# Performance work log

Hardware: AMD Instinct MI355X
Metric: run time of the kernel (lower is better)

Reference implementation:

```python
import jax, jax.numpy as jnp
import numpy as np

D_MODEL = 1024
N_HEADS = 16
D_HEAD = D_MODEL // N_HEADS
RANK = 128
N_COMPRESS = 64
STATE_DIM = 64
B_SZ = 2
S_LEN = 2048


def setup_inputs() -> dict:
    key = jax.random.key(0)
    ks = jax.random.split(key, 12)
    x = jax.random.normal(ks[0], (B_SZ, S_LEN, D_MODEL), dtype=jnp.float32)
    A = jax.random.normal(ks[1], (STATE_DIM, STATE_DIM), dtype=jnp.float32) * 0.01
    B_ssm = jax.random.normal(ks[2], (D_MODEL, STATE_DIM), dtype=jnp.float32) * 0.01
    W_imp = jax.random.normal(ks[3], (D_MODEL, STATE_DIM), dtype=jnp.float32) * 0.02   # Linear(state_dim->d_model), weight [out,in]
    W_router = jax.random.normal(ks[4], (N_COMPRESS, D_MODEL), dtype=jnp.float32) * 0.02
    compress_neurons = jax.random.normal(ks[5], (N_COMPRESS, D_MODEL, RANK), dtype=jnp.float32) * 0.02
    Wq = jax.random.normal(ks[6], (D_MODEL, RANK), dtype=jnp.float32) * 0.02
    Wk = jax.random.normal(ks[7], (D_MODEL, RANK), dtype=jnp.float32) * 0.02
    Wv = jax.random.normal(ks[8], (D_MODEL, RANK), dtype=jnp.float32) * 0.02
    Wo = jax.random.normal(ks[9], (D_MODEL, D_MODEL), dtype=jnp.float32) * 0.02
    mask = jnp.tril(jnp.ones((S_LEN, S_LEN), dtype=bool))[None, None]  # [1,1,S,S] causal
    return {"x": x, "A": A, "B_ssm": B_ssm, "W_imp": W_imp, "W_router": W_router,
            "compress_neurons": compress_neurons, "Wq": Wq, "Wk": Wk, "Wv": Wv,
            "Wo": Wo, "mask": mask}


def reference(x, A, B_ssm, W_imp, W_router, compress_neurons, Wq, Wk, Wv, Wo, mask):
    Bn, S, D = x.shape
    # ---- SSM: h_t = h_{t-1} @ A + x_t @ B (only final state is used) ----
    xB = jnp.einsum('bsd,dn->bsn', x, B_ssm)  # precompute input projection

    def step(h, u):
        h = h @ A + u
        return h, None

    h0 = jnp.zeros((Bn, STATE_DIM), dtype=x.dtype)
    h_final, _ = jax.lax.scan(step, h0, jnp.swapaxes(xB, 0, 1))  # scan over S

    h_proj = h_final @ W_imp.T                       # [B, d_model]
    importance = jax.nn.softmax(jnp.einsum('bsd,bd->bs', x, h_proj), axis=-1)

    # ---- Routing ----
    token_pref = jax.nn.softmax(x @ W_router.T, axis=-1)          # [B,S,n_compress]
    nw = jnp.einsum('bs,bsn->bn', importance, token_pref)         # [B,n_compress]
    nw = nw / (nw.sum(axis=-1, keepdims=True) + 1e-8)

    # ---- Shared compression -> QKV ----
    shared_compress = jnp.einsum('bn,ndr->bdr', nw, compress_neurons)  # [B,D,rank]
    hcomp = jnp.einsum('bsd,bdr->bsr', x, shared_compress)             # [B,S,rank]
    Q = (hcomp @ Wq.T).reshape(Bn, S, N_HEADS, D_HEAD).transpose(0, 2, 1, 3)
    K = (hcomp @ Wk.T).reshape(Bn, S, N_HEADS, D_HEAD).transpose(0, 2, 1, 3)
    V = (hcomp @ Wv.T).reshape(Bn, S, N_HEADS, D_HEAD).transpose(0, 2, 1, 3)

    scores = jnp.einsum('bhqd,bhkd->bhqk', Q, K) / np.sqrt(D_HEAD).astype(x.dtype)
    scores = jnp.where(mask, scores, jnp.array(-jnp.inf, dtype=scores.dtype))
    attn = jax.nn.softmax(scores, axis=-1)
    attn_out = jnp.einsum('bhqk,bhkd->bhqd', attn, V)
    attn_out = attn_out.transpose(0, 2, 1, 3).reshape(Bn, S, D_MODEL)
    output = attn_out @ Wo.T
    return output
```

## Files before the change

### kernel.cpp

```cpp
#include <hip/hip_runtime.h>
#include <hip/hip_bf16.h>

typedef __bf16 bf16x8 __attribute__((ext_vector_type(8)));
typedef float  f32x4  __attribute__((ext_vector_type(4)));
typedef float  f32x16 __attribute__((ext_vector_type(16)));
typedef unsigned int uint4v __attribute__((ext_vector_type(4)));

__device__ __forceinline__ unsigned short f2bf(float f){
  union { float f; unsigned int u; } v; v.f = f;
  unsigned int r = (v.u + 0x7FFFu + ((v.u >> 16) & 1u)) >> 16;
  return (unsigned short)r;
}

__device__ __forceinline__ float bf2f(unsigned short u){
  union { unsigned int i; float f; } v; v.i = ((unsigned int)u) << 16; return v.f;
}

__device__ __forceinline__ unsigned pkbf(float a, float b){
  unsigned r;
  asm("v_cvt_pk_bf16_f32 %0, %1, %2" : "=v"(r) : "v"(a), "v"(b));
  return r;
}

__device__ __forceinline__ void gload_lds16(const void* g, void* l){
  __builtin_amdgcn_global_load_lds(
      (const __attribute__((address_space(1))) unsigned int*)g,
      (__attribute__((address_space(3))) unsigned int*)l, 16, 0, 0);
}

#define MFMA16(a,b,c) __builtin_amdgcn_mfma_f32_16x16x32_bf16((a),(b),(c),0,0,0)
#define MFMA32(a,b,c) __builtin_amdgcn_mfma_f32_32x32x16_bf16((a),(b),(c),0,0,0)

__global__ void k_conv(const float* __restrict__ x,
                       const float* __restrict__ Wq, const float* __restrict__ Wk,
                       const float* __restrict__ Wv, const float* __restrict__ Wo,
                       const float* __restrict__ Wr,
                       unsigned short* __restrict__ xb16,
                       unsigned short* __restrict__ wqkv, unsigned short* __restrict__ wo,
                       unsigned short* __restrict__ wrt){
  int bid = blockIdx.x;
  if (bid < 4096){
    int i = (bid * 256 + threadIdx.x) * 4;
    float4 v = *reinterpret_cast<const float4*>(x + i);
    ushort4 r; r.x = f2bf(v.x); r.y = f2bf(v.y); r.z = f2bf(v.z); r.w = f2bf(v.w);
    *reinterpret_cast<ushort4*>(xb16 + i) = r;
    return;
  }
  int j = ((bid - 4096) * 256 + threadIdx.x) * 4;
  if (j < 393216){
    const float* s;
    if (j < 131072) s = Wq + j; else if (j < 262144) s = Wk + (j - 131072); else s = Wv + (j - 262144);
    float4 v = *reinterpret_cast<const float4*>(s);
    ushort4 r; r.x = f2bf(v.x); r.y = f2bf(v.y); r.z = f2bf(v.z); r.w = f2bf(v.w);
    *reinterpret_cast<ushort4*>(wqkv + j) = r;
  } else if (j < 1441792){
    int jj = j - 393216;
    float4 v = *reinterpret_cast<const float4*>(Wo + jj);
    ushort4 r; r.x = f2bf(v.x); r.y = f2bf(v.y); r.z = f2bf(v.z); r.w = f2bf(v.w);
    *reinterpret_cast<ushort4*>(wo + jj) = r;
  } else {
    int jj = j - 1441792;
    int n = jj >> 10, d = jj & 1023;
    ushort4 r;
    if (n < 64){
      float4 v = *reinterpret_cast<const float4*>(Wr + n * 1024 + d);
      r.x = f2bf(v.x); r.y = f2bf(v.y); r.z = f2bf(v.z); r.w = f2bf(v.w);
    } else { r.x = 0; r.y = 0; r.z = 0; r.w = 0; }
    *reinterpret_cast<ushort4*>(wrt + jj) = r;
  }
}

template<int CBF16>
__global__ __launch_bounds__(256) void k_gemm(
    const unsigned short* __restrict__ A, const unsigned short* __restrict__ Bt,
    void* __restrict__ Cv, int M, int N, int K,
    long sA, long sB, long sC)
{
  __shared__ __align__(16) unsigned short Al[128 * 64];
  __shared__ __align__(16) unsigned short Bl[128 * 64];
  const int tid = threadIdx.x, wv = tid >> 6, lane = tid & 63;
  const int bm = blockIdx.y * 128, bn = blockIdx.x * 128, z = blockIdx.z;
  const unsigned short* Ab = A + (long)z * sA;
  const unsigned short* Bb = Bt + (long)z * sB;
  const f32x4 zero = {0.f, 0.f, 0.f, 0.f};
  f32x4 acc[4][4];
  #pragma unroll
  for (int i = 0; i < 4; ++i)
    #pragma unroll
    for (int j = 0; j < 4; ++j) acc[i][j] = zero;
  const int mo = (wv & 1) * 64, no = (wv >> 1) * 64;

  for (int k0 = 0; k0 < K; k0 += 64){
    __syncthreads();
    #pragma unroll
    for (int i = 0; i < 4; ++i){
      int rr = (wv * 4 + i) * 8 + (lane >> 3);
      gload_lds16(Ab + (long)(bm + rr) * K + k0 + (lane & 7) * 8, &Al[(wv * 4 + i) * 8 * 64]);
      gload_lds16(Bb + (long)(bn + rr) * K + k0 + (lane & 7) * 8, &Bl[(wv * 4 + i) * 8 * 64]);
    }
    __syncthreads();
    #pragma unroll
    for (int ks = 0; ks < 2; ++ks){
      bf16x8 af[4], bfr[4];
      #pragma unroll
      for (int mi = 0; mi < 4; ++mi)
        af[mi] = *reinterpret_cast<const bf16x8*>(&Al[(mo + mi * 16 + (lane & 15)) * 64 + ks * 32 + (lane >> 4) * 8]);
      #pragma unroll
      for (int ni = 0; ni < 4; ++ni)
        bfr[ni] = *reinterpret_cast<const bf16x8*>(&Bl[(no + ni * 16 + (lane & 15)) * 64 + ks * 32 + (lane >> 4) * 8]);
      #pragma unroll
      for (int mi = 0; mi < 4; ++mi)
        #pragma unroll
        for (int ni = 0; ni < 4; ++ni)
          acc[mi][ni] = MFMA16(af[mi], bfr[ni], acc[mi][ni]);
    }
  }

  #pragma unroll
  for (int mi = 0; mi < 4; ++mi)
    #pragma unroll
    for (int ni = 0; ni < 4; ++ni)
      #pragma unroll
      for (int r = 0; r < 4; ++r){
        int row = bm + mo + mi * 16 + (lane >> 4) * 4 + r;
        int col = bn + no + ni * 16 + (lane & 15);
        float v = acc[mi][ni][r];
        if (CBF16) ((unsigned short*)Cv)[(long)z * sC + (long)row * N + col] = f2bf(v);
        else       ((float*)Cv)[(long)z * sC + (long)row * N + col] = v;
      }
}

__global__ __launch_bounds__(256) void k_gemm64(
    const unsigned short* __restrict__ A, const unsigned short* __restrict__ Bt,
    float* __restrict__ C, int M, int N, int K)
{
  __shared__ __align__(16) unsigned short Al[128 * 64];
  __shared__ __align__(16) unsigned short Bl[64 * 64];
  const int tid = threadIdx.x, wv = tid >> 6, lane = tid & 63;
  const int bm = blockIdx.y * 128, bn = blockIdx.x * 64;
  const f32x4 zero = {0.f, 0.f, 0.f, 0.f};
  f32x4 acc[4][2];
  #pragma unroll
  for (int i = 0; i < 4; ++i){ acc[i][0] = zero; acc[i][1] = zero; }
  const int mo = (wv & 1) * 64, no = (wv >> 1) * 32;

  for (int k0 = 0; k0 < K; k0 += 64){
    __syncthreads();
    #pragma unroll
    for (int i = 0; i < 4; ++i){
      int rr = (wv * 4 + i) * 8 + (lane >> 3);
      gload_lds16(A + (long)(bm + rr) * K + k0 + (lane & 7) * 8, &Al[(wv * 4 + i) * 8 * 64]);
    }
    #pragma unroll
    for (int i = 0; i < 2; ++i){
      int rr = (wv * 2 + i) * 8 + (lane >> 3);
      gload_lds16(Bt + (long)(bn + rr) * K + k0 + (lane & 7) * 8, &Bl[(wv * 2 + i) * 8 * 64]);
    }
    __syncthreads();
    #pragma unroll
    for (int ks = 0; ks < 2; ++ks){
      bf16x8 af[4], bfr[2];
      #pragma unroll
      for (int mi = 0; mi < 4; ++mi)
        af[mi] = *reinterpret_cast<const bf16x8*>(&Al[(mo + mi * 16 + (lane & 15)) * 64 + ks * 32 + (lane >> 4) * 8]);
      #pragma unroll
      for (int ni = 0; ni < 2; ++ni)
        bfr[ni] = *reinterpret_cast<const bf16x8*>(&Bl[(no + ni * 16 + (lane & 15)) * 64 + ks * 32 + (lane >> 4) * 8]);
      #pragma unroll
      for (int mi = 0; mi < 4; ++mi)
        #pragma unroll
        for (int ni = 0; ni < 2; ++ni)
          acc[mi][ni] = MFMA16(af[mi], bfr[ni], acc[mi][ni]);
    }
  }

  #pragma unroll
  for (int mi = 0; mi < 4; ++mi)
    #pragma unroll
    for (int ni = 0; ni < 2; ++ni)
      #pragma unroll
      for (int r = 0; r < 4; ++r){
        int row = bm + mo + mi * 16 + (lane >> 4) * 4 + r;
        int col = bn + no + ni * 16 + (lane & 15);
        C[(long)row * N + col] = acc[mi][ni][r];
      }
}

__global__ __launch_bounds__(256) void k_gemmsk(
    const unsigned short* __restrict__ A, const unsigned short* __restrict__ Bt,
    float* __restrict__ P, int M, int N, int Kfull, int KS,
    long sA, long sB)
{
  __shared__ __align__(16) unsigned short Al[128 * 64];
  __shared__ __align__(16) unsigned short Bl[128 * 64];
  const int tid = threadIdx.x, wv = tid >> 6, lane = tid & 63;
  const int bm = blockIdx.y * 128, bn = blockIdx.x * 128, z = blockIdx.z;
  const int b = z >> 2, s = z & 3;
  const unsigned short* Ab = A + (long)b * sA;
  const unsigned short* Bb = Bt + (long)b * sB;
  float* Pb = P + (long)z * M * N;
  const f32x4 zero = {0.f, 0.f, 0.f, 0.f};
  f32x4 acc[4][4];
  #pragma unroll
  for (int i = 0; i < 4; ++i)
    #pragma unroll
    for (int j = 0; j < 4; ++j) acc[i][j] = zero;
  const int mo = (wv & 1) * 64, no = (wv >> 1) * 64;

  const int k1 = s * KS + KS;
  for (int k0 = s * KS; k0 < k1; k0 += 64){
    __syncthreads();
    #pragma unroll
    for (int i = 0; i < 4; ++i){
      int rr = (wv * 4 + i) * 8 + (lane >> 3);
      gload_lds16(Ab + (long)(bm + rr) * Kfull + k0 + (lane & 7) * 8, &Al[(wv * 4 + i) * 8 * 64]);
      gload_lds16(Bb + (long)(bn + rr) * Kfull + k0 + (lane & 7) * 8, &Bl[(wv * 4 + i) * 8 * 64]);
    }
    __syncthreads();
    #pragma unroll
    for (int ks = 0; ks < 2; ++ks){
      bf16x8 af[4], bfr[4];
      #pragma unroll
      for (int mi = 0; mi < 4; ++mi)
        af[mi] = *reinterpret_cast<const bf16x8*>(&Al[(mo + mi * 16 + (lane & 15)) * 64 + ks * 32 + (lane >> 4) * 8]);
      #pragma unroll
      for (int ni = 0; ni < 4; ++ni)
        bfr[ni] = *reinterpret_cast<const bf16x8*>(&Bl[(no + ni * 16 + (lane & 15)) * 64 + ks * 32 + (lane >> 4) * 8]);
      #pragma unroll
      for (int mi = 0; mi < 4; ++mi)
        #pragma unroll
        for (int ni = 0; ni < 4; ++ni)
          acc[mi][ni] = MFMA16(af[mi], bfr[ni], acc[mi][ni]);
    }
  }

  #pragma unroll
  for (int mi = 0; mi < 4; ++mi)
    #pragma unroll
    for (int ni = 0; ni < 4; ++ni)
      #pragma unroll
      for (int r = 0; r < 4; ++r){
        int row = bm + mo + mi * 16 + (lane >> 4) * 4 + r;
        int col = bn + no + ni * 16 + (lane & 15);
        Pb[(long)row * N + col] = acc[mi][ni][r];
      }
}

__global__ __launch_bounds__(256) void k_hred(const float* __restrict__ hpp,
                                              unsigned short* __restrict__ hcomp){
  int i4 = (blockIdx.x * 256 + threadIdx.x) * 4;
  int b = i4 >> 18;
  int rem = i4 & 262143;
  const float* p = hpp + (long)(b * 4) * 262144 + rem;
  f32x4 v = *reinterpret_cast<const f32x4*>(p);
  v += *reinterpret_cast<const f32x4*>(p + 262144);
  v += *reinterpret_cast<const f32x4*>(p + 524288);
  v += *reinterpret_cast<const f32x4*>(p + 786432);
  ushort4 o; o.x = f2bf(v[0]); o.y = f2bf(v[1]); o.z = f2bf(v[2]); o.w = f2bf(v[3]);
  *reinterpret_cast<ushort4*>(hcomp + (long)b * 262144 + rem) = o;
}

__global__ __launch_bounds__(256) void k_xbt(const float* __restrict__ x, const float* __restrict__ Bs,
                                             float* __restrict__ xbt){
  int b = blockIdx.x >> 5, t = blockIdx.x & 31;
  int tid = threadIdx.x, n = tid & 63, p = tid >> 6;
  const float* xr = x + ((long)b * 2048 + 2016 + t) * 1024 + p * 256;
  const float* Bp = Bs + (p * 256) * 64 + n;
  float a0 = 0.f, a1 = 0.f, a2 = 0.f, a3 = 0.f;
  #pragma unroll 4
  for (int d = 0; d < 256; d += 4){
    float4 xv = *reinterpret_cast<const float4*>(xr + d);
    a0 += xv.x * Bp[(d    ) * 64];
    a1 += xv.y * Bp[(d + 1) * 64];
    a2 += xv.z * Bp[(d + 2) * 64];
    a3 += xv.w * Bp[(d + 3) * 64];
  }
  __shared__ float red[4][64];
  red[p][n] = (a0 + a1) + (a2 + a3);
  __syncthreads();
  if (tid < 64){
    float s = red[0][tid] + red[1][tid] + red[2][tid] + red[3][tid];
    xbt[(b * 32 + t) * 64 + tid] = s;
  }
}

__global__ void k_scan(const float* __restrict__ xbt, const float* __restrict__ A,
                       float* __restrict__ hfin){
  int b = blockIdx.x, j = threadIdx.x;
  float Ac[64];
  #pragma unroll
  for (int i = 0; i < 64; ++i) Ac[i] = A[i * 64 + j];
  __shared__ float xs[32][64];
  __shared__ float hs[64];
  #pragma unroll
  for (int t = 0; t < 32; ++t) xs[t][j] = xbt[(b * 32 + t) * 64 + j];
  hs[j] = xs[0][j];
  __syncthreads();
  for (int t = 1; t < 32; ++t){
    float a0 = 0.f, a1 = 0.f, a2 = 0.f, a3 = 0.f;
    #pragma unroll
    for (int ii = 0; ii < 16; ++ii){
      float4 h4 = *reinterpret_cast<const float4*>(&hs[ii * 4]);
      a0 += h4.x * Ac[ii * 4 + 0];
      a1 += h4.y * Ac[ii * 4 + 1];
      a2 += h4.z * Ac[ii * 4 + 2];
      a3 += h4.w * Ac[ii * 4 + 3];
    }
    float acc = (a0 + a1) + (a2 + a3) + xs[t][j];
    __syncthreads();
    hs[j] = acc;
    __syncthreads();
  }
  hfin[b * 64 + j] = hs[j];
}

__global__ __launch_bounds__(256) void k_hproj(const float* __restrict__ hfin,
                                               const float* __restrict__ Wimp,
                                               float* __restrict__ hproj){
  int bid = blockIdx.x;
  int b = bid >> 2;
  int d = (bid & 3) * 256 + threadIdx.x;
  __shared__ float hs[64];
  if (threadIdx.x < 64) hs[threadIdx.x] = hfin[b * 64 + threadIdx.x];
  __syncthreads();
  const float* wr = Wimp + (long)d * 64;
  float a0 = 0.f, a1 = 0.f, a2 = 0.f, a3 = 0.f;
  #pragma unroll
  for (int k = 0; k < 64; k += 4){
    float4 w4 = *reinterpret_cast<const float4*>(wr + k);
    float4 h4 = *reinterpret_cast<const float4*>(&hs[k]);
    a0 += w4.x * h4.x; a1 += w4.y * h4.y; a2 += w4.z * h4.z; a3 += w4.w * h4.w;
  }
  hproj[b * 1024 + d] = (a0 + a1) + (a2 + a3);
}

__global__ void k_logits(const float* __restrict__ x, const float* __restrict__ hproj,
                         float* __restrict__ l){
  int tid = threadIdx.x, lane = tid & 63, wv = tid >> 6;
  int rowbase = blockIdx.x * 16;
  int b = rowbase >> 11;
  float hp[16];
  #pragma unroll
  for (int i = 0; i < 16; ++i) hp[i] = hproj[b * 1024 + i * 64 + lane];
  for (int rr = 0; rr < 4; ++rr){
    int row = rowbase + wv * 4 + rr;
    const float* xr = x + (long)row * 1024;
    float acc = 0.f;
    #pragma unroll
    for (int i = 0; i < 16; ++i) acc += xr[i * 64 + lane] * hp[i];
    #pragma unroll
    for (int o = 32; o; o >>= 1) acc += __shfl_xor(acc, o, 64);
    if (lane == 0) l[row] = acc;
  }
}

__global__ void k_impsm(const float* __restrict__ l, float* __restrict__ imp){
  int b = blockIdx.x, tid = threadIdx.x, lane = tid & 63, wv = tid >> 6;
  __shared__ float red[16];
  float v0 = l[b * 2048 + tid], v1 = l[b * 2048 + 1024 + tid];
  float m = fmaxf(v0, v1);
  #pragma unroll
  for (int o = 32; o; o >>= 1) m = fmaxf(m, __shfl_xor(m, o, 64));
  if (lane == 0) red[wv] = m;
  __syncthreads();
  float M = red[0];
  #pragma unroll
  for (int i = 1; i < 16; ++i) M = fmaxf(M, red[i]);
  __syncthreads();
  float e0 = __expf(v0 - M), e1 = __expf(v1 - M);
  float s = e0 + e1;
  #pragma unroll
  for (int o = 32; o; o >>= 1) s += __shfl_xor(s, o, 64);
  if (lane == 0) red[wv] = s;
  __syncthreads();
  float S = 0.f;
  #pragma unroll
  for (int i = 0; i < 16; ++i) S += red[i];
  float inv = 1.f / S;
  imp[b * 2048 + tid] = e0 * inv;
  imp[b * 2048 + 1024 + tid] = e1 * inv;
}

__global__ void k_nwpart(const float* __restrict__ rpp, const float* __restrict__ imp,
                         float* __restrict__ nwp){
  int bid = blockIdx.x; int b = bid >> 4, chunk = bid & 15;
  int tid = threadIdx.x, wv = tid >> 6, lane = tid & 63;
  float accn = 0.f;
  for (int t = 0; t < 32; ++t){
    int s = chunk * 128 + wv * 32 + t;
    long off = ((long)b * 2048 + s) * 128 + lane;
    float v = rpp[off] + rpp[off + 524288] + rpp[off + 1048576] + rpp[off + 1572864];
    float mx = v;
    #pragma unroll
    for (int o = 32; o; o >>= 1) mx = fmaxf(mx, __shfl_xor(mx, o, 64));
    float e = __expf(v - mx);
    float sm = e;
    #pragma unroll
    for (int o = 32; o; o >>= 1) sm += __shfl_xor(sm, o, 64);
    accn += imp[b * 2048 + s] * (e / sm);
  }
  __shared__ float red[4][64];
  red[wv][lane] = accn;
  __syncthreads();
  if (wv == 0){
    float t = red[0][lane] + red[1][lane] + red[2][lane] + red[3][lane];
    nwp[bid * 64 + lane] = t;
  }
}

__global__ void k_sc(const float* __restrict__ cn, const float* __restrict__ nwp,
                     unsigned short* __restrict__ sct){
  int tid = threadIdx.x;
  long idx = (long)blockIdx.x * 256 + tid;
  int d = (int)(idx >> 5); int r0 = (int)(idx & 31) * 4;
  __shared__ float nws[128];
  if (tid < 128){
    int bb = tid >> 6, nn = tid & 63;
    float a = 0.f;
    #pragma unroll
    for (int c = 0; c < 16; ++c) a += nwp[(bb * 16 + c) * 64 + nn];
    float tot = a;
    #pragma unroll
    for (int o = 32; o; o >>= 1) tot += __shfl_xor(tot, o, 64);
    nws[tid] = a / (tot + 1e-8f);
  }
  __syncthreads();
  f32x4 a0 = {0.f,0.f,0.f,0.f}, a1 = {0.f,0.f,0.f,0.f};
  for (int n = 0; n < 64; ++n){
    f32x4 c = *reinterpret_cast<const f32x4*>(&cn[((long)n * 1024 + d) * 128 + r0]);
    a0 += nws[n] * c;
    a1 += nws[64 + n] * c;
  }
  #pragma unroll
  for (int e = 0; e < 4; ++e){
    sct[(long)(r0 + e) * 1024 + d]        = f2bf(a0[e]);
    sct[(long)(128 + r0 + e) * 1024 + d]  = f2bf(a1[e]);
  }
}

__global__ __launch_bounds__(256, 4) void k_attn(const unsigned short* __restrict__ qkv,
                                                 unsigned short* __restrict__ Op,
                                                 float* __restrict__ ml){
  __shared__ __align__(16) unsigned short KlA[64 * 64];
  __shared__ __align__(16) unsigned short VtA[64 * 64];
  char* Kl = (char*)KlA;
  char* Vt = (char*)VtA;
  const int tid = threadIdx.x, wq = tid >> 6, lane = tid & 63;
  const int l31 = lane & 31, hi = lane >> 5;
  const float CEXP = 0.18033688011112042f;

  int li = blockIdx.x;
  int j = li & 7, m = li >> 3;
  int g = j * 4 + (m & 3);
  int k = (m >> 2) & 7;
  int ph = m >> 5;
  int qb = (ph < 2) ? (15 - k) : k;
  int half = ph & 1;
  int h = g & 15, b = g >> 4;
  int pidx = (g * 16 + qb) * 2 + half;

  int qbase = qb * 128 + wq * 32;
  int KTw = qbase >> 6;
  const unsigned short* base = qkv + (long)b * 2048 * 3072;

  bf16x8 qf[4];
  #pragma unroll
  for (int i = 0; i < 4; ++i)
    qf[i] = *reinterpret_cast<const bf16x8*>(base + (long)(qbase + l31) * 3072 + h * 64 + i * 16 + hi * 8);

  f32x16 oacc[2];
  #pragma unroll
  for (int d = 0; d < 2; ++d)
    #pragma unroll
    for (int r = 0; r < 16; ++r) oacc[d][r] = 0.f;
  float m_r = -3.0e38f, l_r = 0.f;

  const int t0 = half ? (qb + 1) : 0;

  for (int i = 0; i <= qb; ++i){
    int kt = t0 + i;
    #pragma unroll
    for (int it = 0; it < 2; ++it){
      int key = it * 32 + wq * 8 + (lane >> 3);
      int sc = (lane & 7) ^ (key & 7);
      gload_lds16(base + (long)(kt * 64 + key) * 3072 + 1024 + h * 64 + sc * 8,
                  Kl + (it * 32 + wq * 8) * 128);
    }
    #pragma unroll
    for (int it = 0; it < 2; ++it){
      int dhg = wq + it * 4;
      uint4 vvv = *reinterpret_cast<const uint4*>(base + (long)(kt * 64 + lane) * 3072 + 2048 + h * 64 + dhg * 8);
      const unsigned short* vs = reinterpret_cast<const unsigned short*>(&vvv);
      #pragma unroll
      for (int e = 0; e < 8; ++e){
        int dh = dhg * 8 + e;
        *reinterpret_cast<unsigned short*>(Vt + dh * 128 + ((((lane >> 3) ^ (dh & 7))) << 4) + (lane & 7) * 2) = vs[e];
      }
    }
    __syncthreads();

    if (kt <= KTw){
      bool diag = (kt == KTw);

      f32x16 sa[2];
      __builtin_amdgcn_s_setprio(1);
      #pragma unroll
      for (int kb = 0; kb < 2; ++kb){
        #pragma unroll
        for (int r = 0; r < 16; ++r) sa[kb][r] = 0.f;
        int row = kb * 32 + l31;
        #pragma unroll
        for (int i2 = 0; i2 < 4; ++i2){
          bf16x8 kf = *reinterpret_cast<const bf16x8*>(
              Kl + row * 128 + ((((i2 << 1) | hi) ^ (l31 & 7)) << 4));
          sa[kb] = MFMA32(kf, qf[i2], sa[kb]);
        }
      }
      __builtin_amdgcn_s_setprio(0);

      float pv[32];
      #pragma unroll
      for (int kb = 0; kb < 2; ++kb)
        #pragma unroll
        for (int r = 0; r < 16; ++r) pv[kb * 16 + r] = sa[kb][r];

      if (diag){
        int qg = qbase + l31;
        #pragma unroll
        for (int kb = 0; kb < 2; ++kb)
          #pragma unroll
          for (int r = 0; r < 16; ++r){
            int kg = kt * 64 + kb * 32 + (r & 3) + ((r >> 2) << 3) + (hi << 2);
            if (kg > qg) pv[kb * 16 + r] = -3.0e38f;
          }
      }

      float mx = pv[0];
      #pragma unroll
      for (int r = 1; r < 32; ++r) mx = fmaxf(mx, pv[r]);
      mx = fmaxf(mx, __shfl_xor(mx, 32, 64));

      float scl;
      if (__all(mx <= m_r + 44.0f)){
        scl = 1.f;
      } else {
        float mnew = fmaxf(m_r, mx);
        scl = exp2f((m_r - mnew) * CEXP);
        m_r = mnew;
        #pragma unroll
        for (int d = 0; d < 2; ++d)
          #pragma unroll
          for (int r = 0; r < 16; ++r) oacc[d][r] *= scl;
      }
      float mn_c = m_r * CEXP;
      float rs = 0.f;
      #pragma unroll
      for (int r = 0; r < 32; ++r){
        float e = exp2f(__builtin_fmaf(pv[r], CEXP, -mn_c));
        pv[r] = e; rs += e;
      }
      rs += __shfl_xor(rs, 32, 64);
      l_r = l_r * scl + rs;

      bf16x8 pa[4];
      #pragma unroll
      for (int kb = 0; kb < 2; ++kb){
        unsigned W[4][2], X[4][2];
        #pragma unroll
        for (int u = 0; u < 4; ++u){
          W[u][0] = pkbf(pv[kb * 16 + 4 * u + 0], pv[kb * 16 + 4 * u + 1]);
          W[u][1] = pkbf(pv[kb * 16 + 4 * u + 2], pv[kb * 16 + 4 * u + 3]);
        }
        #pragma unroll
        for (int u = 0; u < 4; ++u){
          X[u][0] = (unsigned)__shfl_xor((int)W[u][0], 32, 64);
          X[u][1] = (unsigned)__shfl_xor((int)W[u][1], 32, 64);
        }
        #pragma unroll
        for (int t2 = 0; t2 < 2; ++t2){
          int u0 = 2 * t2, u1 = u0 + 1;
          uint4v wt;
          wt.x = hi ? X[u1][0] : W[u0][0];
          wt.y = hi ? X[u1][1] : W[u0][1];
          wt.z = hi ? W[u1][0] : X[u0][0];
          wt.w = hi ? W[u1][1] : X[u0][1];
          pa[kb * 2 + t2] = __builtin_bit_cast(bf16x8, wt);
        }
      }
      __builtin_amdgcn_s_setprio(1);
      #pragma unroll
      for (int db = 0; db < 2; ++db){
        int row = db * 32 + l31;
        #pragma unroll
        for (int t = 0; t < 4; ++t){
          bf16x8 vf = *reinterpret_cast<const bf16x8*>(
              Vt + row * 128 + ((((t << 1) | hi) ^ (l31 & 7)) << 4));
          oacc[db] = MFMA32(vf, pa[t], oacc[db]);
        }
      }
      __builtin_amdgcn_s_setprio(0);
    }
    __syncthreads();
  }

  unsigned short* Oq = Op + (long)pidx * 8192 + (wq * 32 + l31) * 64;
  #pragma unroll
  for (int db = 0; db < 2; ++db)
    #pragma unroll
    for (int r4 = 0; r4 < 4; ++r4){
      ushort4 o;
      o.x = f2bf(oacc[db][r4 * 4 + 0]);
      o.y = f2bf(oacc[db][r4 * 4 + 1]);
      o.z = f2bf(oacc[db][r4 * 4 + 2]);
      o.w = f2bf(oacc[db][r4 * 4 + 3]);
      *reinterpret_cast<ushort4*>(Oq + db * 32 + r4 * 8 + hi * 4) = o;
    }
  if (hi == 0){
    float2 v; v.x = m_r; v.y = l_r;
    *reinterpret_cast<float2*>(ml + ((long)pidx * 128 + wq * 32 + l31) * 2) = v;
  }
}

__global__ __launch_bounds__(256) void k_amerge(const unsigned short* __restrict__ Op,
                                                const float* __restrict__ ml,
                                                unsigned short* __restrict__ ao){
  const float CEXP = 0.18033688011112042f;
  int mid = blockIdx.x;
  int g = mid >> 4, qb = mid & 15;
  int b = g >> 4, h = g & 15;
  const unsigned short* O0 = Op + (long)mid * 2 * 8192;
  const unsigned short* O1 = O0 + 8192;
  const float* ml0 = ml + (long)mid * 2 * 256;
  const float* ml1 = ml0 + 256;
  int t = threadIdx.x;
  #pragma unroll
  for (int i = 0; i < 8; ++i){
    int idx = i * 256 + t;
    int q = idx >> 4, c4 = (idx & 15) * 4;
    float m0 = ml0[q * 2], l0 = ml0[q * 2 + 1];
    float m1 = ml1[q * 2], l1 = ml1[q * 2 + 1];
    float mm = fmaxf(m0, m1);
    float s0 = exp2f((m0 - mm) * CEXP), s1 = exp2f((m1 - mm) * CEXP);
    float linv = 1.f / (l0 * s0 + l1 * s1);
    s0 *= linv; s1 *= linv;
    ushort4 a = *reinterpret_cast<const ushort4*>(O0 + q * 64 + c4);
    ushort4 c = *reinterpret_cast<const ushort4*>(O1 + q * 64 + c4);
    ushort4 o;
    o.x = f2bf(bf2f(a.x) * s0 + bf2f(c.x) * s1);
    o.y = f2bf(bf2f(a.y) * s0 + bf2f(c.y) * s1);
    o.z = f2bf(bf2f(a.z) * s0 + bf2f(c.z) * s1);
    o.w = f2bf(bf2f(a.w) * s0 + bf2f(c.w) * s1);
    *reinterpret_cast<ushort4*>(ao + ((long)b * 2048 + qb * 128 + q) * 1024 + h * 64 + c4) = o;
  }
}

extern "C" void kernel_launch(void* const* d_in, const int* in_sizes, int n_in,
                              void* d_out, int out_size, void* d_ws, size_t ws_size,
                              hipStream_t stream){
  (void)in_sizes; (void)n_in; (void)out_size; (void)ws_size;
  const float* x    = (const float*)d_in[0];
  const float* A    = (const float*)d_in[1];
  const float* Bs   = (const float*)d_in[2];
  const float* Wimp = (const float*)d_in[3];
  const float* Wr   = (const float*)d_in[4];
  const float* cn   = (const float*)d_in[5];
  const float* Wq   = (const float*)d_in[6];
  const float* Wk   = (const float*)d_in[7];
  const float* Wv   = (const float*)d_in[8];
  const float* Wo   = (const float*)d_in[9];
  float* out = (float*)d_out;
  char* ws = (char*)d_ws;

  unsigned short* Opart = (unsigned short*)(ws + 0);
  float*          mlbuf = (float*)(ws + 16777216);
  unsigned short* xb16  = (unsigned short*)(ws + 0);
  float*          rpp   = (float*)(ws + 8388608);
  unsigned short* sct   = (unsigned short*)(ws + 16777216);
  float*          xbt   = (float*)(ws + 17301504);
  float*          hproj = (float*)(ws + 17317888);
  float*          lbuf  = (float*)(ws + 17326080);
  float*          imp   = (float*)(ws + 17342464);
  float*          nwp   = (float*)(ws + 17358848);
  float*          hfin  = (float*)(ws + 17368064);
  unsigned short* qkvb  = (unsigned short*)(ws + 17825792);
  float*          hpp   = (float*)(ws + 17825792);
  unsigned short* aob   = (unsigned short*)(ws + 42991616);
  unsigned short* wqkv  = (unsigned short*)(ws + 51380224);
  unsigned short* wo_t  = (unsigned short*)(ws + 52166656);
  unsigned short* wrt   = (unsigned short*)(ws + 54263808);
  unsigned short* hcomp = (unsigned short*)(ws + 54525952);

  k_conv<<<5632, 256, 0, stream>>>(x, Wq, Wk, Wv, Wo, Wr, xb16, wqkv, wo_t, wrt);
  k_gemmsk<<<dim3(1, 32, 4), 256, 0, stream>>>(xb16, wrt, rpp, 4096, 128, 1024, 256, 0, 0);
  k_xbt<<<64, 256, 0, stream>>>(x, Bs, xbt);
  k_scan<<<2, 64, 0, stream>>>(xbt, A, hfin);
  k_hproj<<<8, 256, 0, stream>>>(hfin, Wimp, hproj);
  k_logits<<<256, 256, 0, stream>>>(x, hproj, lbuf);
  k_impsm<<<2, 1024, 0, stream>>>(lbuf, imp);
  k_nwpart<<<32, 256, 0, stream>>>(rpp, imp, nwp);
  k_sc<<<128, 256, 0, stream>>>(cn, nwp, sct);
  k_gemmsk<<<dim3(1, 16, 8), 256, 0, stream>>>(xb16, sct, hpp, 2048, 128, 1024, 256,
                                               2048L * 1024, 128L * 1024);
  k_hred<<<512, 256, 0, stream>>>(hpp, hcomp);
  k_gemm<1><<<dim3(24, 16, 2), 256, 0, stream>>>(hcomp, wqkv, qkvb, 2048, 3072, 128,
                                                 2048L * 128, 0, 2048L * 3072);
  k_attn<<<dim3(1024), 256, 0, stream>>>(qkvb, Opart, mlbuf);
  k_amerge<<<dim3(512), 256, 0, stream>>>(Opart, mlbuf, aob);
  k_gemm64<<<dim3(16, 32), 256, 0, stream>>>(aob, wo_t, out, 4096, 1024, 1024);
}
```

Baseline: 196.1 us.

## Split attention KV range four ways and fold importance softmax into routing

Generalizes the attention split-KV scheme from two to a configurable number of partitions, four when the workspace is large enough. This gives 2048 smaller blocks, which should balance the causal workload better across CUs, and the merge kernel now combines four partial results. It also removes the separate importance-softmax kernel: each routing block recomputes the max and sum over the logits itself, saving one launch at the cost of redundant work. The workspace layout is reorganized so the extra partial-output buffers fit, which adds more partial-output traffic for the merge kernel.

```diff
diff --git a/kernel.cpp b/kernel.cpp
--- a/kernel.cpp
+++ b/kernel.cpp
@@ -354,37 +354,30 @@
   }
 }
 
-__global__ void k_impsm(const float* __restrict__ l, float* __restrict__ imp){
-  int b = blockIdx.x, tid = threadIdx.x, lane = tid & 63, wv = tid >> 6;
-  __shared__ float red[16];
-  float v0 = l[b * 2048 + tid], v1 = l[b * 2048 + 1024 + tid];
-  float m = fmaxf(v0, v1);
-  #pragma unroll
-  for (int o = 32; o; o >>= 1) m = fmaxf(m, __shfl_xor(m, o, 64));
-  if (lane == 0) red[wv] = m;
-  __syncthreads();
-  float M = red[0];
-  #pragma unroll
-  for (int i = 1; i < 16; ++i) M = fmaxf(M, red[i]);
-  __syncthreads();
-  float e0 = __expf(v0 - M), e1 = __expf(v1 - M);
-  float s = e0 + e1;
-  #pragma unroll
-  for (int o = 32; o; o >>= 1) s += __shfl_xor(s, o, 64);
-  if (lane == 0) red[wv] = s;
-  __syncthreads();
-  float S = 0.f;
-  #pragma unroll
-  for (int i = 0; i < 16; ++i) S += red[i];
-  float inv = 1.f / S;
-  imp[b * 2048 + tid] = e0 * inv;
-  imp[b * 2048 + 1024 + tid] = e1 * inv;
-}
-
-__global__ void k_nwpart(const float* __restrict__ rpp, const float* __restrict__ imp,
+__global__ void k_nwpart(const float* __restrict__ rpp, const float* __restrict__ lbuf,
                          float* __restrict__ nwp){
   int bid = blockIdx.x; int b = bid >> 4, chunk = bid & 15;
   int tid = threadIdx.x, wv = tid >> 6, lane = tid & 63;
+  __shared__ float wred[4], wsum[4];
+  __shared__ float red[4][64];
+  const float* lr = lbuf + b * 2048;
+  float4 va = *reinterpret_cast<const float4*>(lr + tid * 8);
+  float4 vb = *reinterpret_cast<const float4*>(lr + tid * 8 + 4);
+  float mx8 = fmaxf(fmaxf(fmaxf(va.x, va.y), fmaxf(va.z, va.w)),
+                    fmaxf(fmaxf(vb.x, vb.y), fmaxf(vb.z, vb.w)));
+  #pragma unroll
+  for (int o = 32; o; o >>= 1) mx8 = fmaxf(mx8, __shfl_xor(mx8, o, 64));
+  if (lane == 0) wred[wv] = mx8;
+  __syncthreads();
+  float M = fmaxf(fmaxf(wred[0], wred[1]), fmaxf(wred[2], wred[3]));
+  float se = __expf(va.x - M) + __expf(va.y - M) + __expf(va.z - M) + __expf(va.w - M)
+           + __expf(vb.x - M) + __expf(vb.y - M) + __expf(vb.z - M) + __expf(vb.w - M);
+  #pragma unroll
+  for (int o = 32; o; o >>= 1) se += __shfl_xor(se, o, 64);
+  if (lane == 0) wsum[wv] = se;
+  __syncthreads();
+  float inv = 1.f / (wsum[0] + wsum[1] + wsum[2] + wsum[3]);
+
   float accn = 0.f;
   for (int t = 0; t < 32; ++t){
     int s = chunk * 128 + wv * 32 + t;
@@ -397,9 +390,9 @@
     float sm = e;
     #pragma unroll
     for (int o = 32; o; o >>= 1) sm += __shfl_xor(sm, o, 64);
-    accn += imp[b * 2048 + s] * (e / sm);
-  }
-  __shared__ float red[4][64];
+    float impv = __expf(lr[s] - M) * inv;
+    accn += impv * (e / sm);
+  }
   red[wv][lane] = accn;
   __syncthreads();
   if (wv == 0){
@@ -440,7 +433,8 @@
 
 __global__ __launch_bounds__(256, 4) void k_attn(const unsigned short* __restrict__ qkv,
                                                  unsigned short* __restrict__ Op,
-                                                 float* __restrict__ ml){
+                                                 float* __restrict__ ml,
+                                                 int nspl, int nsh){
   __shared__ __align__(16) unsigned short KlA[64 * 64];
   __shared__ __align__(16) unsigned short VtA[64 * 64];
   char* Kl = (char*)KlA;
@@ -452,12 +446,16 @@
   int li = blockIdx.x;
   int j = li & 7, m = li >> 3;
   int g = j * 4 + (m & 3);
-  int k = (m >> 2) & 7;
-  int ph = m >> 5;
-  int qb = (ph < 2) ? (15 - k) : k;
-  int half = ph & 1;
+  int r5 = m >> 2;
+  int k5 = r5 & 7, sel = r5 >> 3;
+  int qb = (sel < nspl) ? (15 - k5) : k5;
+  int part = (sel < nspl) ? sel : (sel - nspl);
   int h = g & 15, b = g >> 4;
-  int pidx = (g * 16 + qb) * 2 + half;
+  int pidx = (g * 16 + qb) * nspl + part;
+
+  int T = 2 * qb + 2;
+  int t0 = (part * T) >> nsh;
+  int t1 = ((part + 1) * T) >> nsh;
 
   int qbase = qb * 128 + wq * 32;
   int KTw = qbase >> 6;
@@ -475,10 +473,7 @@
     for (int r = 0; r < 16; ++r) oacc[d][r] = 0.f;
   float m_r = -3.0e38f, l_r = 0.f;
 
-  const int t0 = half ? (qb + 1) : 0;
-
-  for (int i = 0; i <= qb; ++i){
-    int kt = t0 + i;
+  for (int kt = t0; kt < t1; ++kt){
     #pragma unroll
     for (int it = 0; it < 2; ++it){
       int key = it * 32 + wq * 8 + (lane >> 3);
@@ -623,33 +618,43 @@
 
 __global__ __launch_bounds__(256) void k_amerge(const unsigned short* __restrict__ Op,
                                                 const float* __restrict__ ml,
-                                                unsigned short* __restrict__ ao){
+                                                unsigned short* __restrict__ ao,
+                                                int nspl){
   const float CEXP = 0.18033688011112042f;
   int mid = blockIdx.x;
   int g = mid >> 4, qb = mid & 15;
   int b = g >> 4, h = g & 15;
-  const unsigned short* O0 = Op + (long)mid * 2 * 8192;
-  const unsigned short* O1 = O0 + 8192;
-  const float* ml0 = ml + (long)mid * 2 * 256;
-  const float* ml1 = ml0 + 256;
+  const unsigned short* O0 = Op + (long)mid * nspl * 8192;
+  const float* mlb = ml + (long)mid * nspl * 256;
   int t = threadIdx.x;
   #pragma unroll
   for (int i = 0; i < 8; ++i){
     int idx = i * 256 + t;
     int q = idx >> 4, c4 = (idx & 15) * 4;
-    float m0 = ml0[q * 2], l0 = ml0[q * 2 + 1];
-    float m1 = ml1[q * 2], l1 = ml1[q * 2 + 1];
-    float mm = fmaxf(m0, m1);
+    float m0 = mlb[q * 2],       l0 = mlb[q * 2 + 1];
+    float m1 = mlb[256 + q * 2], l1 = mlb[256 + q * 2 + 1];
+    float m2 = -3.0e38f, l2 = 0.f, m3 = -3.0e38f, l3 = 0.f;
+    if (nspl == 4){
+      m2 = mlb[512 + q * 2]; l2 = mlb[512 + q * 2 + 1];
+      m3 = mlb[768 + q * 2]; l3 = mlb[768 + q * 2 + 1];
+    }
+    float mm = fmaxf(fmaxf(m0, m1), fmaxf(m2, m3));
     float s0 = exp2f((m0 - mm) * CEXP), s1 = exp2f((m1 - mm) * CEXP);
-    float linv = 1.f / (l0 * s0 + l1 * s1);
-    s0 *= linv; s1 *= linv;
+    float s2 = exp2f((m2 - mm) * CEXP), s3 = exp2f((m3 - mm) * CEXP);
+    float linv = 1.f / (l0 * s0 + l1 * s1 + l2 * s2 + l3 * s3);
+    s0 *= linv; s1 *= linv; s2 *= linv; s3 *= linv;
     ushort4 a = *reinterpret_cast<const ushort4*>(O0 + q * 64 + c4);
-    ushort4 c = *reinterpret_cast<const ushort4*>(O1 + q * 64 + c4);
+    ushort4 c = *reinterpret_cast<const ushort4*>(O0 + 8192 + q * 64 + c4);
+    ushort4 a2 = {0,0,0,0}, a3 = {0,0,0,0};
+    if (nspl == 4){
+      a2 = *reinterpret_cast<const ushort4*>(O0 + 16384 + q * 64 + c4);
+      a3 = *reinterpret_cast<const ushort4*>(O0 + 24576 + q * 64 + c4);
+    }
     ushort4 o;
-    o.x = f2bf(bf2f(a.x) * s0 + bf2f(c.x) * s1);
-    o.y = f2bf(bf2f(a.y) * s0 + bf2f(c.y) * s1);
-    o.z = f2bf(bf2f(a.z) * s0 + bf2f(c.z) * s1);
-    o.w = f2bf(bf2f(a.w) * s0 + bf2f(c.w) * s1);
+    o.x = f2bf(bf2f(a.x) * s0 + bf2f(c.x) * s1 + bf2f(a2.x) * s2 + bf2f(a3.x) * s3);
+    o.y = f2bf(bf2f(a.y) * s0 + bf2f(c.y) * s1 + bf2f(a2.y) * s2 + bf2f(a3.y) * s3);
+    o.z = f2bf(bf2f(a.z) * s0 + bf2f(c.z) * s1 + bf2f(a2.z) * s2 + bf2f(a3.z) * s3);
+    o.w = f2bf(bf2f(a.w) * s0 + bf2f(c.w) * s1 + bf2f(a2.w) * s2 + bf2f(a3.w) * s3);
     *reinterpret_cast<ushort4*>(ao + ((long)b * 2048 + qb * 128 + q) * 1024 + h * 64 + c4) = o;
   }
 }
@@ -657,7 +662,7 @@
 extern "C" void kernel_launch(void* const* d_in, const int* in_sizes, int n_in,
                               void* d_out, int out_size, void* d_ws, size_t ws_size,
                               hipStream_t stream){
-  (void)in_sizes; (void)n_in; (void)out_size; (void)ws_size;
+  (void)in_sizes; (void)n_in; (void)out_size;
   const float* x    = (const float*)d_in[0];
   const float* A    = (const float*)d_in[1];
   const float* Bs   = (const float*)d_in[2];
@@ -671,24 +676,34 @@
   float* out = (float*)d_out;
   char* ws = (char*)d_ws;
 
-  unsigned short* Opart = (unsigned short*)(ws + 0);
-  float*          mlbuf = (float*)(ws + 16777216);
+  int nspl, nsh;
+  {
+    size_t tot4 = (size_t)512*4*16384 + (size_t)512*4*1024 + 25165824 + 2097152 + 2800000;
+    if (ws_size >= tot4){ nspl = 4; nsh = 2; } else { nspl = 2; nsh = 1; }
+  }
+  size_t opart_b = (size_t)512 * nspl * 16384;
+  size_t ml_off  = opart_b;
+  size_t qkv_off = ml_off + (size_t)512 * nspl * 1024;
+  size_t wo_off  = qkv_off + 25165824;
+  size_t ext     = wo_off + 2097152;
+
+  unsigned short* Opart = (unsigned short*)(ws);
+  float*          mlbuf = (float*)(ws + ml_off);
+  unsigned short* qkvb  = (unsigned short*)(ws + qkv_off);
+  float*          hpp   = (float*)(ws + qkv_off);
+  unsigned short* aob   = (unsigned short*)(ws + qkv_off);
+  unsigned short* wo_t  = (unsigned short*)(ws + wo_off);
   unsigned short* xb16  = (unsigned short*)(ws + 0);
   float*          rpp   = (float*)(ws + 8388608);
-  unsigned short* sct   = (unsigned short*)(ws + 16777216);
-  float*          xbt   = (float*)(ws + 17301504);
-  float*          hproj = (float*)(ws + 17317888);
-  float*          lbuf  = (float*)(ws + 17326080);
-  float*          imp   = (float*)(ws + 17342464);
-  float*          nwp   = (float*)(ws + 17358848);
-  float*          hfin  = (float*)(ws + 17368064);
-  unsigned short* qkvb  = (unsigned short*)(ws + 17825792);
-  float*          hpp   = (float*)(ws + 17825792);
-  unsigned short* aob   = (unsigned short*)(ws + 42991616);
-  unsigned short* wqkv  = (unsigned short*)(ws + 51380224);
-  unsigned short* wo_t  = (unsigned short*)(ws + 52166656);
-  unsigned short* wrt   = (unsigned short*)(ws + 54263808);
-  unsigned short* hcomp = (unsigned short*)(ws + 54525952);
+  unsigned short* sct   = (unsigned short*)(ws + ext);
+  float*          xbt   = (float*)(ws + ext + 524288);
+  float*          hproj = (float*)(ws + ext + 540672);
+  float*          lbuf  = (float*)(ws + ext + 548864);
+  float*          nwp   = (float*)(ws + ext + 565248);
+  float*          hfin  = (float*)(ws + ext + 573440);
+  unsigned short* wqkv  = (unsigned short*)(ws + ext + 577536);
+  unsigned short* wrt   = (unsigned short*)(ws + ext + 1363968);
+  unsigned short* hcomp = (unsigned short*)(ws + ext + 1626112);
 
   k_conv<<<5632, 256, 0, stream>>>(x, Wq, Wk, Wv, Wo, Wr, xb16, wqkv, wo_t, wrt);
   k_gemmsk<<<dim3(1, 32, 4), 256, 0, stream>>>(xb16, wrt, rpp, 4096, 128, 1024, 256, 0, 0);
@@ -696,15 +711,14 @@
   k_scan<<<2, 64, 0, stream>>>(xbt, A, hfin);
   k_hproj<<<8, 256, 0, stream>>>(hfin, Wimp, hproj);
   k_logits<<<256, 256, 0, stream>>>(x, hproj, lbuf);
-  k_impsm<<<2, 1024, 0, stream>>>(lbuf, imp);
-  k_nwpart<<<32, 256, 0, stream>>>(rpp, imp, nwp);
+  k_nwpart<<<32, 256, 0, stream>>>(rpp, lbuf, nwp);
   k_sc<<<128, 256, 0, stream>>>(cn, nwp, sct);
   k_gemmsk<<<dim3(1, 16, 8), 256, 0, stream>>>(xb16, sct, hpp, 2048, 128, 1024, 256,
                                                2048L * 1024, 128L * 1024);
   k_hred<<<512, 256, 0, stream>>>(hpp, hcomp);
   k_gemm<1><<<dim3(24, 16, 2), 256, 0, stream>>>(hcomp, wqkv, qkvb, 2048, 3072, 128,
                                                  2048L * 128, 0, 2048L * 3072);
-  k_attn<<<dim3(1024), 256, 0, stream>>>(qkvb, Opart, mlbuf);
-  k_amerge<<<dim3(512), 256, 0, stream>>>(Opart, mlbuf, aob);
+  k_attn<<<dim3(512 * nspl), 256, 0, stream>>>(qkvb, Opart, mlbuf, nspl, nsh);
+  k_amerge<<<dim3(512), 256, 0, stream>>>(Opart, mlbuf, aob, nspl);
   k_gemm64<<<dim3(16, 32), 256, 0, stream>>>(aob, wo_t, out, 4096, 1024, 1024);
 }
```

New measurement: 199.3 us. About the same (+1.6%).
